# Kernel optimization log

Hardware: AMD Instinct MI355X
Metric: run time of the kernel (lower is better)

Reference implementation:

```python
import jax, jax.numpy as jnp
import numpy as np

NS = 16   # scalar multiplicity (ns)
NV = 4    # vector multiplicity (nv)
N_EDGE_FEAT = 3 * NS          # 48
W_NUMEL = NS * NS + NS * NV   # 320 = fully-connected TP weight numel


def setup_inputs() -> dict:
    key = jax.random.key(0)
    ks = jax.random.split(key, 8)
    N, E = 50000, 600000
    node_attr = jax.random.normal(ks[0], (N, NS), jnp.float32)          # 16x0e node features
    edge_index = jax.random.randint(ks[1], (2, E), 0, N)                # [src; dst]
    edge_attr = jax.random.normal(ks[2], (E, NS), jnp.float32)          # embedded edge attr (ns)
    edge_sh = jax.random.normal(ks[3], (E, 9), jnp.float32)             # sh lmax=2: 1+3+5
    s = 0.05
    fc1_w = jax.random.normal(ks[4], (N_EDGE_FEAT, N_EDGE_FEAT), jnp.float32) * s
    fc1_b = jnp.zeros((N_EDGE_FEAT,), jnp.float32)
    fc2_w = jax.random.normal(ks[5], (N_EDGE_FEAT, W_NUMEL), jnp.float32) * s
    fc2_b = jnp.zeros((W_NUMEL,), jnp.float32)
    return {"node_attr": node_attr, "edge_attr": edge_attr, "edge_sh": edge_sh,
            "fc1_w": fc1_w, "fc1_b": fc1_b, "fc2_w": fc2_w, "fc2_b": fc2_b,
            "edge_index": edge_index}


def reference(node_attr, edge_attr, edge_sh, fc1_w, fc1_b, fc2_w, fc2_b, edge_index):
    """TensorProductConvLayer forward: gather -> per-edge weighted tensor product -> scatter-mean.
    in_irreps=16x0e, sh=1x0e+1x1o+1x2e, out_irreps=16x0e+4x1o (residual=False, batch_norm=False)."""
    src, dst = edge_index[0], edge_index[1]
    E = edge_attr.shape[0]
    N = node_attr.shape[0]
    # edge feature = cat(edge_attr, scalar node feats of src and dst)  -> [E, 48]
    ea = jnp.concatenate([edge_attr, node_attr[src], node_attr[dst]], axis=-1)
    # fc MLP -> per-edge tensor-product weights [E, 320]
    h = jax.nn.relu(ea @ fc1_w + fc1_b)
    w = h @ fc2_w + fc2_b
    w0 = w[:, : NS * NS].reshape(E, NS, NS)   # path 0e x 0e -> 0e
    w1 = w[:, NS * NS :].reshape(E, NS, NV)   # path 0e x 1o -> 1o
    x = node_attr[dst]                        # gathered scalar features [E, 16]
    inv = 1.0 / jnp.sqrt(jnp.float32(NS))     # e3nn path normalization (fan-in = 16)
    sh0 = edge_sh[:, :1]                      # l=0 component
    sh1 = edge_sh[:, 1:4]                     # l=1 components
    out0 = jnp.einsum('eu,euw->ew', x * sh0, w0) * inv           # [E, 16]
    out1 = jnp.einsum('eu,em,euw->ewm', x, sh1, w1) * inv        # [E, 4, 3]
    msg = jnp.concatenate([out0, out1.reshape(E, NV * 3)], axis=-1)  # [E, 28]
    # scatter-mean to source nodes
    summed = jax.ops.segment_sum(msg, src, num_segments=N)
    cnt = jax.ops.segment_sum(jnp.ones((E, 1), msg.dtype), src, num_segments=N)
    return summed / jnp.maximum(cnt, 1.0)
```

## Files before the change

### kernel.cpp

```cpp
#include <hip/hip_runtime.h>

#define NS   16
#define NV   4
#define FEAT 48
#define WN   320
#define MSG  28
#define MSGB 32

typedef __bf16 bf16x8 __attribute__((ext_vector_type(8)));
typedef __bf16 bf16x4 __attribute__((ext_vector_type(4)));
typedef float  f32x4  __attribute__((ext_vector_type(4)));

#define PK1_ELEMS (2 * 3 * 64 * 8)
#define PK2_ELEMS (2 * 20 * 64 * 8)
#define PACK_BLOCKS 8

__global__ void prep_kernel(const float* __restrict__ fc1_w, const float* __restrict__ fc1_b,
                            const float* __restrict__ fc2_w, const float* __restrict__ fc2_b,
                            const int* __restrict__ src,
                            __bf16* __restrict__ pk1, __bf16* __restrict__ pk2,
                            int* __restrict__ count, int E)
{
    const int tid = threadIdx.x;
    if (blockIdx.x < PACK_BLOCKS) {
        const int idx = blockIdx.x * 256 + tid;
        const int stride = PACK_BLOCKS * 256;
        for (int i = idx; i < PK1_ELEMS; i += stride) {
            const int j = i & 7, l = (i >> 3) & 63, f = i >> 9;
            const int nt = f % 3, p = f / 3;
            const int q = l >> 4, col = 16 * nt + (l & 15);
            float v;
            if (p == 0) {
                const int k = (j < 4) ? (4 * q + j) : (16 + 4 * q + j - 4);
                v = fc1_w[k * FEAT + col];
            } else if (j < 4) {
                v = fc1_w[(32 + 4 * q + j) * FEAT + col];
            } else {
                v = (j == 4 && q == 0) ? fc1_b[col] : 0.f;
            }
            pk1[i] = (__bf16)v;
        }
        for (int i = idx; i < PK2_ELEMS; i += stride) {
            const int j = i & 7, l = (i >> 3) & 63, f = i >> 9;
            const int nt = f % 20, p = f / 20;
            const int q = l >> 4, col = 16 * nt + (l & 15);
            float v;
            if (p == 0) {
                const int k = (j < 4) ? (4 * q + j) : (16 + 4 * q + j - 4);
                v = fc2_w[k * WN + col];
            } else if (j < 4) {
                v = fc2_w[(32 + 4 * q + j) * WN + col];
            } else {
                v = (j == 4 && q == 0) ? fc2_b[col] : 0.f;
            }
            pk2[i] = (__bf16)v;
        }
    } else {
        const int nb = gridDim.x - PACK_BLOCKS;
        for (int e = (blockIdx.x - PACK_BLOCKS) * 256 + tid; e < E; e += nb * 256)
            atomicAdd(&count[src[e]], 1);
    }
}

__global__ void scan_block(const int* __restrict__ in, int* __restrict__ outExcl,
                           int* __restrict__ bsum, int n)
{
    __shared__ int s[256];
    const int tid = threadIdx.x;
    const int i = blockIdx.x * 256 + tid;
    int v = (i < n) ? in[i] : 0;
    int acc = v;
    s[tid] = acc;
    __syncthreads();
    #pragma unroll
    for (int off = 1; off < 256; off <<= 1) {
        int t = (tid >= off) ? s[tid - off] : 0;
        __syncthreads();
        acc += t;
        s[tid] = acc;
        __syncthreads();
    }
    if (i < n) outExcl[i] = acc - v;
    if (tid == 255) bsum[blockIdx.x] = acc;
}

__global__ void fill_rank(const int* __restrict__ src,
                          const int* __restrict__ base, const int* __restrict__ boff,
                          int* __restrict__ cursor, int* __restrict__ rank, int E)
{
    const int e = blockIdx.x * blockDim.x + threadIdx.x;
    if (e < E) {
        const int s = src[e];
        const int pos = atomicAdd(&cursor[s], 1);
        rank[e] = base[s] + boff[s >> 8] + pos;
    }
}

template<int MODE>
__global__ __launch_bounds__(256, 6) void edge_mfma_kernel(
    const float* __restrict__ node_attr,
    const float* __restrict__ edge_attr,
    const float* __restrict__ edge_sh,
    const int*   __restrict__ edge_index,
    const int*   __restrict__ rank,
    const __bf16* __restrict__ pk1,
    const __bf16* __restrict__ pk2,
    __bf16* __restrict__ msg,
    float*  __restrict__ out_acc,
    float*  __restrict__ cnt,
    int E)
{
    __shared__ float sX[4][32][20];

    const int tid = threadIdx.x;
    const int w   = tid >> 6;
    const int l   = tid & 63;
    const int q   = l >> 4;
    const int r16 = l & 15;
    const int e0  = (blockIdx.x * 4 + w) * 32;

    const float4 z4 = make_float4(0.f, 0.f, 0.f, 0.f);
    const float bias1 = (q == 0) ? 1.f : 0.f;

    bf16x8 w1f[2][3];
    #pragma unroll
    for (int p = 0; p < 2; ++p)
        #pragma unroll
        for (int nt = 0; nt < 3; ++nt)
            w1f[p][nt] = *reinterpret_cast<const bf16x8*>(pk1 + ((size_t)(p * 3 + nt) * 64 + l) * 8);

    bf16x8 eaf[2][2];
    int   dstI[2], srcI[2], rnkI[2];
    bool  evt[2];
    float sh0[2], sh1[2];
    #pragma unroll
    for (int t = 0; t < 2; ++t) {
        const int e = e0 + 16 * t + r16;
        const bool ev = (e < E);
        evt[t] = ev;
        srcI[t] = ev ? edge_index[e] : 0;
        dstI[t] = ev ? edge_index[E + e] : 0;
        rnkI[t] = (MODE == 0 && ev) ? rank[e] : 0;
        float4 ea4 = z4, sa4 = z4, da4 = z4;
        if (ev) {
            ea4 = *reinterpret_cast<const float4*>(edge_attr + (size_t)e * NS + 4 * q);
            sa4 = *reinterpret_cast<const float4*>(node_attr + (size_t)srcI[t] * NS + 4 * q);
            da4 = *reinterpret_cast<const float4*>(node_attr + (size_t)dstI[t] * NS + 4 * q);
        }
        *reinterpret_cast<f32x4*>(&sX[w][16 * t + r16][4 * q]) =
            f32x4{da4.x, da4.y, da4.z, da4.w};

        bf16x8 f0, f1;
        f0[0]=(__bf16)ea4.x; f0[1]=(__bf16)ea4.y; f0[2]=(__bf16)ea4.z; f0[3]=(__bf16)ea4.w;
        f0[4]=(__bf16)sa4.x; f0[5]=(__bf16)sa4.y; f0[6]=(__bf16)sa4.z; f0[7]=(__bf16)sa4.w;
        f1[0]=(__bf16)da4.x; f1[1]=(__bf16)da4.y; f1[2]=(__bf16)da4.z; f1[3]=(__bf16)da4.w;
        f1[4]=(__bf16)bias1; f1[5]=(__bf16)0.f; f1[6]=(__bf16)0.f; f1[7]=(__bf16)0.f;
        eaf[t][0] = f0;
        eaf[t][1] = f1;
        sh0[t] = ev ? edge_sh[(size_t)e * 9] : 0.f;
        sh1[t] = (ev && q < 3) ? edge_sh[(size_t)e * 9 + 1 + q] : 0.f;
    }

    bf16x8 hc[2][2];
    #pragma unroll
    for (int t = 0; t < 2; ++t) {
        f32x4 h0 = {0.f,0.f,0.f,0.f}, h1 = {0.f,0.f,0.f,0.f}, h2 = {0.f,0.f,0.f,0.f};
        h0 = __builtin_amdgcn_mfma_f32_16x16x32_bf16(w1f[0][0], eaf[t][0], h0, 0, 0, 0);
        h0 = __builtin_amdgcn_mfma_f32_16x16x32_bf16(w1f[1][0], eaf[t][1], h0, 0, 0, 0);
        h1 = __builtin_amdgcn_mfma_f32_16x16x32_bf16(w1f[0][1], eaf[t][0], h1, 0, 0, 0);
        h1 = __builtin_amdgcn_mfma_f32_16x16x32_bf16(w1f[1][1], eaf[t][1], h1, 0, 0, 0);
        h2 = __builtin_amdgcn_mfma_f32_16x16x32_bf16(w1f[0][2], eaf[t][0], h2, 0, 0, 0);
        h2 = __builtin_amdgcn_mfma_f32_16x16x32_bf16(w1f[1][2], eaf[t][1], h2, 0, 0, 0);
        bf16x8 c0, c1;
        #pragma unroll
        for (int g = 0; g < 4; ++g) {
            c0[g]     = (__bf16)fmaxf(h0[g], 0.f);
            c0[4 + g] = (__bf16)fmaxf(h1[g], 0.f);
            c1[g]     = (__bf16)fmaxf(h2[g], 0.f);
        }
        c1[4] = (__bf16)bias1;
        c1[5] = (__bf16)0.f; c1[6] = (__bf16)0.f; c1[7] = (__bf16)0.f;
        hc[t][0] = c0;
        hc[t][1] = c1;
    }

    f32x4 acc0[2] = {{0.f,0.f,0.f,0.f},{0.f,0.f,0.f,0.f}};
    f32x4 acc1[2] = {{0.f,0.f,0.f,0.f},{0.f,0.f,0.f,0.f}};
    #pragma unroll 4
    for (int nt2 = 0; nt2 < 20; ++nt2) {
        const bf16x8 wf0 = *reinterpret_cast<const bf16x8*>(pk2 + ((size_t)(0 * 20 + nt2) * 64 + l) * 8);
        const bf16x8 wf1 = *reinterpret_cast<const bf16x8*>(pk2 + ((size_t)(1 * 20 + nt2) * 64 + l) * 8);
        #pragma unroll
        for (int t = 0; t < 2; ++t) {
            f32x4 d = {0.f,0.f,0.f,0.f};
            d = __builtin_amdgcn_mfma_f32_16x16x32_bf16(wf0, hc[t][0], d, 0, 0, 0);
            d = __builtin_amdgcn_mfma_f32_16x16x32_bf16(wf1, hc[t][1], d, 0, 0, 0);
            if (nt2 < 16) {
                const float xv = sX[w][16 * t + r16][nt2];
                #pragma unroll
                for (int g = 0; g < 4; ++g) acc0[t][g] = fmaf(xv, d[g], acc0[t][g]);
            } else {
                const float xu = sX[w][16 * t + r16][4 * (nt2 - 16) + q];
                #pragma unroll
                for (int g = 0; g < 4; ++g) acc1[t][g] = fmaf(xu, d[g], acc1[t][g]);
            }
        }
    }

    const float inv = 0.25f;

    #pragma unroll
    for (int t = 0; t < 2; ++t)
        #pragma unroll
        for (int g = 0; g < 4; ++g) {
            float s = acc1[t][g];
            s += __shfl_xor(s, 16);
            s += __shfl_xor(s, 32);
            acc1[t][g] = s;
        }

    #pragma unroll
    for (int t = 0; t < 2; ++t) {
        const int e = e0 + 16 * t + r16;
        if (e >= E) continue;
        if (MODE == 0) {
            const size_t mb = (size_t)rnkI[t] * MSGB;
            bf16x4 v4;
            #pragma unroll
            for (int g = 0; g < 4; ++g) v4[g] = (__bf16)(inv * sh0[t] * acc0[t][g]);
            *reinterpret_cast<bf16x4*>(msg + mb + 4 * q) = v4;
            if (q < 3) {
                #pragma unroll
                for (int g = 0; g < 4; ++g)
                    msg[mb + 16 + 3 * g + q] =
                        (__bf16)(inv * sh1[t] * acc1[t][g]);
            }
        } else {
            const size_t ob = (size_t)srcI[t] * MSG;
            #pragma unroll
            for (int g = 0; g < 4; ++g)
                atomicAdd(&out_acc[ob + 4 * q + g], inv * sh0[t] * acc0[t][g]);
            if (q < 3) {
                #pragma unroll
                for (int g = 0; g < 4; ++g)
                    atomicAdd(&out_acc[ob + 16 + 3 * g + q], inv * sh1[t] * acc1[t][g]);
            }
            if (q == 3) atomicAdd(&cnt[srcI[t]], 1.f);
        }
    }
}

__global__ __launch_bounds__(256) void node_reduce(
    const __bf16* __restrict__ msg,
    const int* __restrict__ count,
    const int* __restrict__ base,
    const int* __restrict__ boff,
    float* __restrict__ out, int N)
{
    const int tid  = threadIdx.x;
    const int w    = tid >> 6;
    const int l    = tid & 63;
    const int slot = l >> 5;
    const int c    = l & 31;
    const int n    = blockIdx.x * 8 + w * 2 + slot;
    if (n >= N || c >= MSG) return;

    const int deg = count[n];
    const size_t b = (size_t)(base[n] + boff[n >> 8]) * MSGB;
    float acc = 0.f;
    int j = 0;
    for (; j + 4 <= deg; j += 4) {
        const float v0 = (float)msg[b + (size_t)(j + 0) * MSGB + c];
        const float v1 = (float)msg[b + (size_t)(j + 1) * MSGB + c];
        const float v2 = (float)msg[b + (size_t)(j + 2) * MSGB + c];
        const float v3 = (float)msg[b + (size_t)(j + 3) * MSGB + c];
        acc += (v0 + v1) + (v2 + v3);
    }
    for (; j < deg; ++j) acc += (float)msg[b + (size_t)j * MSGB + c];
    out[(size_t)n * MSG + c] = acc / fmaxf((float)deg, 1.f);
}

__global__ void finalize_kernel(float* __restrict__ out,
                                const float* __restrict__ cnt, int total)
{
    const int idx = blockIdx.x * blockDim.x + threadIdx.x;
    if (idx < total) {
        const int n = idx / MSG;
        out[idx] = out[idx] / fmaxf(cnt[n], 1.0f);
    }
}

extern "C" void kernel_launch(void* const* d_in, const int* in_sizes, int n_in,
                              void* d_out, int out_size, void* d_ws, size_t ws_size,
                              hipStream_t stream)
{
    const float* node_attr  = (const float*)d_in[0];
    const float* edge_attr  = (const float*)d_in[1];
    const float* edge_sh    = (const float*)d_in[2];
    const float* fc1_w      = (const float*)d_in[3];
    const float* fc1_b      = (const float*)d_in[4];
    const float* fc2_w      = (const float*)d_in[5];
    const float* fc2_b      = (const float*)d_in[6];
    const int*   edge_index = (const int*)d_in[7];

    const int N = in_sizes[0] / NS;
    const int E = in_sizes[1] / NS;
    const int nb = (N + 255) / 256;

    char* ws = (char*)d_ws;
    size_t off = 0;
    auto take = [&](size_t bytes) { off = (off + 255) & ~(size_t)255;
                                    size_t o = off; off += bytes; return o; };
    const size_t o_pk1    = take(PK1_ELEMS * 2);
    const size_t o_pk2    = take(PK2_ELEMS * 2);
    const size_t o_count  = take((size_t)N * 4);
    const size_t o_cursor = take((size_t)N * 4);
    const size_t o_base   = take((size_t)N * 4);
    const size_t o_bsum   = take(1024);
    const size_t o_boff   = take(1024);
    const size_t o_tot    = take(1024);
    const size_t o_rank   = take((size_t)E * 4);
    const size_t o_msg    = take((size_t)E * MSGB * 2);
    const bool csr_ok = (off <= ws_size) && (nb <= 256);

    __bf16* pk1 = (__bf16*)(ws + o_pk1);
    __bf16* pk2 = (__bf16*)(ws + o_pk2);
    int* count  = (int*)(ws + o_count);
    float* out  = (float*)d_out;

    const int egrid = (E + 127) / 128;
    const int hblocks = (E + 255) / 256;

    if (csr_ok) {
        int* cursor = (int*)(ws + o_cursor);
        int* base   = (int*)(ws + o_base);
        int* bsum   = (int*)(ws + o_bsum);
        int* boff   = (int*)(ws + o_boff);
        int* tot    = (int*)(ws + o_tot);
        int* rank   = (int*)(ws + o_rank);
        __bf16* msg = (__bf16*)(ws + o_msg);

        hipMemsetAsync(ws + o_count, 0, o_cursor - o_count + (size_t)N * 4, stream);

        prep_kernel<<<PACK_BLOCKS + hblocks, 256, 0, stream>>>(
            fc1_w, fc1_b, fc2_w, fc2_b, edge_index, pk1, pk2, count, E);
        scan_block<<<nb, 256, 0, stream>>>(count, base, bsum, N);
        scan_block<<<1, 256, 0, stream>>>(bsum, boff, tot, nb);
        fill_rank<<<(E + 255) / 256, 256, 0, stream>>>(edge_index, base, boff,
                                                       cursor, rank, E);

        edge_mfma_kernel<0><<<egrid, 256, 0, stream>>>(node_attr, edge_attr, edge_sh,
                                                       edge_index, rank, pk1, pk2,
                                                       msg, nullptr, nullptr, E);

        node_reduce<<<(N + 7) / 8, 256, 0, stream>>>(msg, count, base, boff, out, N);
    } else {
        float* cntp = (float*)(ws + o_cursor);
        hipMemsetAsync(d_out, 0, (size_t)out_size * sizeof(float), stream);
        hipMemsetAsync(ws + o_count, 0, o_cursor - o_count + (size_t)N * 4, stream);
        prep_kernel<<<PACK_BLOCKS + hblocks, 256, 0, stream>>>(
            fc1_w, fc1_b, fc2_w, fc2_b, edge_index, pk1, pk2, count, E);
        edge_mfma_kernel<1><<<egrid, 256, 0, stream>>>(node_attr, edge_attr, edge_sh,
                                                       edge_index, nullptr, pk1, pk2,
                                                       nullptr, out, cntp, E);
        const int total = N * MSG;
        finalize_kernel<<<(total + 255) / 256, 256, 0, stream>>>(out, cntp, total);
    }
}
```

Before: 147.6 us.

## Fuse rank computation into edge MFMA kernel and raise occupancy

Removes the separate fill_rank kernel and its rank buffer. Each edge's slot in the CSR message buffer is now claimed with an atomicAdd inside the edge kernel by the q==0 lane and broadcast to the other lanes with a shuffle. It also raises the launch_bounds occupancy hint from 6 to 8 and wraps the MFMA sequences in s_setprio. This saves one kernel launch and an E-sized write and read of rank, at the cost of atomic latency inside the compute kernel and possible register pressure from the higher occupancy target.

```diff
diff --git a/kernel.cpp b/kernel.cpp
--- a/kernel.cpp
+++ b/kernel.cpp
@@ -84,25 +84,15 @@
     if (tid == 255) bsum[blockIdx.x] = acc;
 }
 
-__global__ void fill_rank(const int* __restrict__ src,
-                          const int* __restrict__ base, const int* __restrict__ boff,
-                          int* __restrict__ cursor, int* __restrict__ rank, int E)
-{
-    const int e = blockIdx.x * blockDim.x + threadIdx.x;
-    if (e < E) {
-        const int s = src[e];
-        const int pos = atomicAdd(&cursor[s], 1);
-        rank[e] = base[s] + boff[s >> 8] + pos;
-    }
-}
-
 template<int MODE>
-__global__ __launch_bounds__(256, 6) void edge_mfma_kernel(
+__global__ __launch_bounds__(256, 8) void edge_mfma_kernel(
     const float* __restrict__ node_attr,
     const float* __restrict__ edge_attr,
     const float* __restrict__ edge_sh,
     const int*   __restrict__ edge_index,
-    const int*   __restrict__ rank,
+    const int*   __restrict__ base,
+    const int*   __restrict__ boff,
+    int*         __restrict__ cursor,
     const __bf16* __restrict__ pk1,
     const __bf16* __restrict__ pk2,
     __bf16* __restrict__ msg,
@@ -130,7 +120,7 @@
             w1f[p][nt] = *reinterpret_cast<const bf16x8*>(pk1 + ((size_t)(p * 3 + nt) * 64 + l) * 8);
 
     bf16x8 eaf[2][2];
-    int   dstI[2], srcI[2], rnkI[2];
+    int   srcI[2], rnkI[2];
     bool  evt[2];
     float sh0[2], sh1[2];
     #pragma unroll
@@ -139,13 +129,20 @@
         const bool ev = (e < E);
         evt[t] = ev;
         srcI[t] = ev ? edge_index[e] : 0;
-        dstI[t] = ev ? edge_index[E + e] : 0;
-        rnkI[t] = (MODE == 0 && ev) ? rank[e] : 0;
+        const int dstI = ev ? edge_index[E + e] : 0;
+
+        int rnk_q0 = 0;
+        if (MODE == 0 && q == 0 && ev) {
+            const int s = srcI[t];
+            rnk_q0 = base[s] + boff[s >> 8] + atomicAdd(&cursor[s], 1);
+        }
+        if (MODE == 0) rnkI[t] = __shfl(rnk_q0, r16);
+
         float4 ea4 = z4, sa4 = z4, da4 = z4;
         if (ev) {
             ea4 = *reinterpret_cast<const float4*>(edge_attr + (size_t)e * NS + 4 * q);
             sa4 = *reinterpret_cast<const float4*>(node_attr + (size_t)srcI[t] * NS + 4 * q);
-            da4 = *reinterpret_cast<const float4*>(node_attr + (size_t)dstI[t] * NS + 4 * q);
+            da4 = *reinterpret_cast<const float4*>(node_attr + (size_t)dstI * NS + 4 * q);
         }
         *reinterpret_cast<f32x4*>(&sX[w][16 * t + r16][4 * q]) =
             f32x4{da4.x, da4.y, da4.z, da4.w};
@@ -165,12 +162,14 @@
     #pragma unroll
     for (int t = 0; t < 2; ++t) {
         f32x4 h0 = {0.f,0.f,0.f,0.f}, h1 = {0.f,0.f,0.f,0.f}, h2 = {0.f,0.f,0.f,0.f};
+        __builtin_amdgcn_s_setprio(1);
         h0 = __builtin_amdgcn_mfma_f32_16x16x32_bf16(w1f[0][0], eaf[t][0], h0, 0, 0, 0);
         h0 = __builtin_amdgcn_mfma_f32_16x16x32_bf16(w1f[1][0], eaf[t][1], h0, 0, 0, 0);
         h1 = __builtin_amdgcn_mfma_f32_16x16x32_bf16(w1f[0][1], eaf[t][0], h1, 0, 0, 0);
         h1 = __builtin_amdgcn_mfma_f32_16x16x32_bf16(w1f[1][1], eaf[t][1], h1, 0, 0, 0);
         h2 = __builtin_amdgcn_mfma_f32_16x16x32_bf16(w1f[0][2], eaf[t][0], h2, 0, 0, 0);
         h2 = __builtin_amdgcn_mfma_f32_16x16x32_bf16(w1f[1][2], eaf[t][1], h2, 0, 0, 0);
+        __builtin_amdgcn_s_setprio(0);
         bf16x8 c0, c1;
         #pragma unroll
         for (int g = 0; g < 4; ++g) {
@@ -193,8 +192,10 @@
         #pragma unroll
         for (int t = 0; t < 2; ++t) {
             f32x4 d = {0.f,0.f,0.f,0.f};
+            __builtin_amdgcn_s_setprio(1);
             d = __builtin_amdgcn_mfma_f32_16x16x32_bf16(wf0, hc[t][0], d, 0, 0, 0);
             d = __builtin_amdgcn_mfma_f32_16x16x32_bf16(wf1, hc[t][1], d, 0, 0, 0);
+            __builtin_amdgcn_s_setprio(0);
             if (nt2 < 16) {
                 const float xv = sX[w][16 * t + r16][nt2];
                 #pragma unroll
@@ -319,7 +320,6 @@
     const size_t o_bsum   = take(1024);
     const size_t o_boff   = take(1024);
     const size_t o_tot    = take(1024);
-    const size_t o_rank   = take((size_t)E * 4);
     const size_t o_msg    = take((size_t)E * MSGB * 2);
     const bool csr_ok = (off <= ws_size) && (nb <= 256);
 
@@ -337,7 +337,6 @@
         int* bsum   = (int*)(ws + o_bsum);
         int* boff   = (int*)(ws + o_boff);
         int* tot    = (int*)(ws + o_tot);
-        int* rank   = (int*)(ws + o_rank);
         __bf16* msg = (__bf16*)(ws + o_msg);
 
         hipMemsetAsync(ws + o_count, 0, o_cursor - o_count + (size_t)N * 4, stream);
@@ -346,12 +345,10 @@
             fc1_w, fc1_b, fc2_w, fc2_b, edge_index, pk1, pk2, count, E);
         scan_block<<<nb, 256, 0, stream>>>(count, base, bsum, N);
         scan_block<<<1, 256, 0, stream>>>(bsum, boff, tot, nb);
-        fill_rank<<<(E + 255) / 256, 256, 0, stream>>>(edge_index, base, boff,
-                                                       cursor, rank, E);
 
         edge_mfma_kernel<0><<<egrid, 256, 0, stream>>>(node_attr, edge_attr, edge_sh,
-                                                       edge_index, rank, pk1, pk2,
-                                                       msg, nullptr, nullptr, E);
+                                                       edge_index, base, boff, cursor,
+                                                       pk1, pk2, msg, nullptr, nullptr, E);
 
         node_reduce<<<(N + 7) / 8, 256, 0, stream>>>(msg, count, base, boff, out, N);
     } else {
@@ -361,8 +358,8 @@
         prep_kernel<<<PACK_BLOCKS + hblocks, 256, 0, stream>>>(
             fc1_w, fc1_b, fc2_w, fc2_b, edge_index, pk1, pk2, count, E);
         edge_mfma_kernel<1><<<egrid, 256, 0, stream>>>(node_attr, edge_attr, edge_sh,
-                                                       edge_index, nullptr, pk1, pk2,
-                                                       nullptr, out, cntp, E);
+                                                       edge_index, nullptr, nullptr, nullptr,
+                                                       pk1, pk2, nullptr, out, cntp, E);
         const int total = N * MSG;
         finalize_kernel<<<(total + 255) / 256, 256, 0, stream>>>(out, cntp, total);
     }
```

Result: no change. 146.5 us (-0.8%).
